# Optimization experiments

Hardware: AMD Instinct MI355X
Metric: run time of the kernel (lower is better)

The kernel has to match this reference:

```python
import math
import jax, jax.numpy as jnp
import numpy as np

B, T, D, L, E = 2, 1024, 1024, 12, 4
EPS = 1e-5


def _ln(v, g, b):
    mu = jnp.mean(v, axis=-1, keepdims=True)
    var = jnp.mean(jnp.square(v - mu), axis=-1, keepdims=True)
    return (v - mu) * jax.lax.rsqrt(var + EPS) * g + b


def setup_inputs() -> dict:
    key = jax.random.key(0)
    ks = jax.random.split(key, 4)
    x = jax.random.normal(ks[0], (B, T, D), dtype=jnp.float32)
    queries = jax.random.normal(ks[1], (L, D), dtype=jnp.float32) * 0.02
    W1 = jax.random.normal(ks[2], (L, D, E * D), dtype=jnp.float32) * 0.02
    W2 = jax.random.normal(ks[3], (L, E * D, D), dtype=jnp.float32) * 0.02
    return {
        'x': x,
        'queries': queries,
        'kn_g': jnp.ones((L, D), jnp.float32),
        'kn_b': jnp.zeros((L, D), jnp.float32),
        'ln_g': jnp.ones((L, D), jnp.float32),
        'ln_b': jnp.zeros((L, D), jnp.float32),
        'W1': W1,
        'b1': jnp.zeros((L, E * D), jnp.float32),
        'W2': W2,
        'b2': jnp.zeros((L, D), jnp.float32),
    }


def reference(x, queries, kn_g, kn_b, ln_g, ln_b, W1, b1, W2, b2):
    scale = 1.0 / math.sqrt(D)
    history = [x]
    h = x
    for l in range(L):
        V = jnp.stack(history, axis=0)              # (l+1, B, T, D)
        K = _ln(V, kn_g[l], kn_b[l])
        scores = jnp.einsum('d,lbtd->lbt', queries[l], K) * scale
        alpha = jax.nn.softmax(scores, axis=0)       # softmax over history axis
        residual = jnp.einsum('lbt,lbtd->btd', alpha, V)
        u = _ln(h, ln_g[l], ln_b[l])
        ff = jax.nn.gelu(u @ W1[l] + b1[l], approximate=False) @ W2[l] + b2[l]
        h = residual + ff
        history.append(h)
    return h
```

## Files before the change

kernel.cpp:

```cpp
#include <hip/hip_runtime.h>
#include <math.h>

#define BATCH 2
#define TSEQ 1024
#define DIM 1024
#define NLAYER 12
#define EDIM 4096
#define BT 2048
#define EPS_LN 1e-5f

typedef __attribute__((ext_vector_type(4))) float  f32x4;
typedef __attribute__((ext_vector_type(8))) __bf16 bf16x8;
typedef __attribute__((ext_vector_type(4))) __bf16 bf16x4;

__device__ __forceinline__ void gl_lds16(const void* gptr, void* lptr) {
    __builtin_amdgcn_global_load_lds(
        (const __attribute__((address_space(1))) void*)gptr,
        (__attribute__((address_space(3))) void*)lptr,
        16, 0, 0);
}

__global__ __launch_bounds__(256)
void attn_kernel(const float* __restrict__ x,
                 const float* __restrict__ hist,
                 const float* __restrict__ q,
                 const float* __restrict__ kng,
                 const float* __restrict__ knb,
                 const float* __restrict__ lng,
                 const float* __restrict__ lnb,
                 const float* __restrict__ b2,
                 float* __restrict__ hnext,
                 __bf16* __restrict__ u,
                 int nl)
{
    __shared__ float V[NLAYER][DIM];
    __shared__ float sS[NLAYER], sMu[NLAYER], sRs[NLAYER];

    const int bt = blockIdx.x;
    const int tid = threadIdx.x, lane = tid & 63, w = tid >> 6;

    f32x4 gqv[4];
    float sg = 0.f, sb = 0.f;
#pragma unroll
    for (int i = 0; i < 4; i++) {
        int d = i * 256 + lane * 4;
        f32x4 g4 = *(const f32x4*)(kng + d);
        f32x4 q4 = *(const f32x4*)(q + d);
        f32x4 b4 = *(const f32x4*)(knb + d);
#pragma unroll
        for (int c = 0; c < 4; c++) {
            float gq = g4[c] * q4[c];
            gqv[i][c] = gq;
            sg += gq;
            sb += b4[c] * q4[c];
        }
    }
#pragma unroll
    for (int off = 32; off; off >>= 1) {
        sg += __shfl_xor(sg, off);
        sb += __shfl_xor(sb, off);
    }

    for (int lp = w; lp < nl; lp += 4) {
        const float* vp = (lp == 0) ? (x + (size_t)bt * DIM)
                                    : (hist + ((size_t)lp * BT + bt) * DIM);
        f32x4 vv[4];
#pragma unroll
        for (int i = 0; i < 4; i++) vv[i] = *(const f32x4*)(vp + i * 256 + lane * 4);
        float s1 = 0.f, s2 = 0.f, sq = 0.f;
#pragma unroll
        for (int i = 0; i < 4; i++) {
            *(f32x4*)(&V[lp][i * 256 + lane * 4]) = vv[i];
#pragma unroll
            for (int c = 0; c < 4; c++) {
                float xv = vv[i][c];
                s1 += xv; s2 += xv * xv; sq += xv * gqv[i][c];
            }
        }
#pragma unroll
        for (int off = 32; off; off >>= 1) {
            s1 += __shfl_xor(s1, off);
            s2 += __shfl_xor(s2, off);
            sq += __shfl_xor(sq, off);
        }
        if (lane == 0) {
            float mu = s1 * (1.0f / DIM);
            float var = s2 * (1.0f / DIM) - mu * mu;
            float rs = rsqrtf(var + EPS_LN);
            sMu[lp] = mu; sRs[lp] = rs;
            sS[lp] = (rs * (sq - mu * sg) + sb) * (1.0f / 32.0f);
        }
    }
    __syncthreads();

    float mx = -1e30f;
#pragma unroll
    for (int i = 0; i < NLAYER; i++) if (i < nl) mx = fmaxf(mx, sS[i]);
    float al[NLAYER];
    float ssum = 0.f;
#pragma unroll
    for (int i = 0; i < NLAYER; i++) {
        al[i] = (i < nl) ? __expf(sS[i] - mx) : 0.f;
        ssum += al[i];
    }
    float inv = 1.0f / ssum;

    const int d = tid * 4;
    f32x4 r; r[0] = 0.f; r[1] = 0.f; r[2] = 0.f; r[3] = 0.f;
#pragma unroll
    for (int i = 0; i < NLAYER; i++) {
        if (i < nl) {
            f32x4 v4 = *(const f32x4*)(&V[i][d]);
            float a = al[i] * inv;
            r[0] += a * v4[0]; r[1] += a * v4[1]; r[2] += a * v4[2]; r[3] += a * v4[3];
        }
    }
    f32x4 h4 = *(const f32x4*)(&V[nl - 1][d]);
    f32x4 b24 = *(const f32x4*)(b2 + d);
    f32x4 ro; ro[0] = r[0] + b24[0]; ro[1] = r[1] + b24[1];
    ro[2] = r[2] + b24[2]; ro[3] = r[3] + b24[3];
    *(f32x4*)(hnext + (size_t)bt * DIM + d) = ro;

    float mu = sMu[nl - 1], rs = sRs[nl - 1];
    f32x4 g4 = *(const f32x4*)(lng + d);
    f32x4 b4 = *(const f32x4*)(lnb + d);
    bf16x4 uo;
#pragma unroll
    for (int c = 0; c < 4; c++) uo[c] = (__bf16)((h4[c] - mu) * rs * g4[c] + b4[c]);
    *(bf16x4*)(u + (size_t)bt * DIM + d) = uo;
}

__global__ __launch_bounds__(256) void wtrans_kernel(
    const float* __restrict__ W1, const float* __restrict__ W2,
    __bf16* __restrict__ W1t, __bf16* __restrict__ W2t)
{
    __shared__ float t[64][65];
    int z = blockIdx.z;
    const float* src; __bf16* dst; int R, C, rt, ct;
    if (z == 0) { src = W1; dst = W1t; R = DIM;  C = EDIM; rt = blockIdx.y; ct = blockIdx.x; }
    else        { src = W2; dst = W2t; R = EDIM; C = DIM;  rt = blockIdx.x; ct = blockIdx.y; }

    int tid = threadIdx.x;
    int lr = tid >> 2, cs = (tid & 3) << 4;
    const float* sp = src + (size_t)(rt * 64 + lr) * C + ct * 64 + cs;
#pragma unroll
    for (int s = 0; s < 4; s++) {
        f32x4 v = *(const f32x4*)(sp + s * 4);
        t[lr][cs + s * 4 + 0] = v[0];
        t[lr][cs + s * 4 + 1] = v[1];
        t[lr][cs + s * 4 + 2] = v[2];
        t[lr][cs + s * 4 + 3] = v[3];
    }
    __syncthreads();
    int oc = tid >> 2, rs = (tid & 3) << 4;
    bf16x8 o0, o1;
#pragma unroll
    for (int e = 0; e < 8; e++) o0[e] = (__bf16)t[rs + e][oc];
#pragma unroll
    for (int e = 0; e < 8; e++) o1[e] = (__bf16)t[rs + 8 + e][oc];
    __bf16* dp = dst + (size_t)(ct * 64 + oc) * R + rt * 64 + rs;
    *(bf16x8*)dp = o0;
    *(bf16x8*)(dp + 8) = o1;
}

#define STG 49152

template <int EPI, int NTN>
__global__ __launch_bounds__(512, 1)
void gemm8(const __bf16* __restrict__ A, const __bf16* __restrict__ Bt,
           const float* __restrict__ bias, float* __restrict__ outp,
           int N, int As, int Bs)
{
    __shared__ char lds[3 * STG];
    const int tid = threadIdx.x, lane = tid & 63, w = tid >> 6;
    const int wm = w >> 2, wn = w & 3;
    const int lr = lane & 15;
    const int hib = (lane >> 4) << 4;
    const int NT = 16;

    const int nb = gridDim.x;
    const int fid = blockIdx.x;
    const int swz = (fid & 7) * (nb >> 3) + (fid >> 3);
    const int m0 = (swz / NTN) * 128;
    const int n0 = (swz % NTN) * 256;
    const int kbase = blockIdx.y * 1024;

    f32x4 acc[4][4];
#pragma unroll
    for (int i = 0; i < 4; i++)
#pragma unroll
        for (int j = 0; j < 4; j++) { acc[i][j][0]=0.f; acc[i][j][1]=0.f; acc[i][j][2]=0.f; acc[i][j][3]=0.f; }

    const int srow = tid >> 3;
    const int ksrc = ((tid & 7) << 4) ^ ((srow & 7) << 4);
    const char* Ac = (const char*)A;
    const char* Bc = (const char*)Bt;
    size_t aoff[2], boff[4];
#pragma unroll
    for (int c = 0; c < 2; c++)
        aoff[c] = ((size_t)(m0 + c * 64 + srow) * As + kbase) * 2 + ksrc;
#pragma unroll
    for (int c = 0; c < 4; c++)
        boff[c] = ((size_t)(n0 + c * 64 + srow) * Bs + kbase) * 2 + ksrc;

    char* abw = lds + w * 1024;
    char* bbw = lds + 16384 + w * 1024;

    auto STAGE = [&](int tt, int bi) {
        size_t kb = (size_t)tt * 128;
        char* ab = abw + bi * STG;
        char* bb = bbw + bi * STG;
#pragma unroll
        for (int c = 0; c < 2; c++) gl_lds16(Ac + aoff[c] + kb, ab + c * 8192);
#pragma unroll
        for (int c = 0; c < 4; c++) gl_lds16(Bc + boff[c] + kb, bb + c * 8192);
    };

    STAGE(0, 0);
    STAGE(1, 1);

    int sb = 0, st = 2;
#pragma unroll 1
    for (int t = 0; t < NT; ++t) {
        if (t < NT - 1) asm volatile("s_waitcnt vmcnt(6)" ::: "memory");
        else            asm volatile("s_waitcnt vmcnt(0)" ::: "memory");
        __builtin_amdgcn_s_barrier();
        __builtin_amdgcn_sched_barrier(0);

        if (t + 2 < NT) STAGE(t + 2, st);

        const char* base = lds + sb * STG;
        bf16x8 af[2][4], bfr[2][4];
#pragma unroll
        for (int kk = 0; kk < 2; kk++) {
#pragma unroll
            for (int i = 0; i < 4; i++) {
                int ra = wm * 64 + i * 16 + lr;
                af[kk][i] = *(const bf16x8*)(base + ra * 128 + ((kk * 64 + hib) ^ ((ra & 7) << 4)));
            }
#pragma unroll
            for (int j = 0; j < 4; j++) {
                int rb = wn * 64 + j * 16 + lr;
                bfr[kk][j] = *(const bf16x8*)(base + 16384 + rb * 128 + ((kk * 64 + hib) ^ ((rb & 7) << 4)));
            }
        }
        __builtin_amdgcn_s_setprio(1);
#pragma unroll
        for (int kk = 0; kk < 2; kk++)
#pragma unroll
            for (int i = 0; i < 4; i++)
#pragma unroll
                for (int j = 0; j < 4; j++)
                    acc[i][j] = __builtin_amdgcn_mfma_f32_16x16x32_bf16(af[kk][i], bfr[kk][j], acc[i][j], 0, 0, 0);
        __builtin_amdgcn_s_setprio(0);

        sb = (sb == 2) ? 0 : sb + 1;
        st = (st == 2) ? 0 : st + 1;
    }

    const int lrow = (lane >> 4) << 2;
    if (EPI == 0) {
        __bf16* out = (__bf16*)outp;
#pragma unroll
        for (int i = 0; i < 4; i++) {
#pragma unroll
            for (int j = 0; j < 4; j++) {
                int colg = n0 + wn * 64 + j * 16 + lr;
                float bc = bias[colg];
#pragma unroll
                for (int r = 0; r < 4; r++) {
                    int rowg = m0 + wm * 64 + i * 16 + lrow + r;
                    float v = acc[i][j][r] + bc;
                    float tt2 = 0.7978845608f * (v + 0.044715f * v * v * v);
                    float e = __expf(2.0f * tt2);
                    float th = 1.0f - 2.0f / (e + 1.0f);
                    out[(size_t)rowg * N + colg] = (__bf16)(0.5f * v * (1.0f + th));
                }
            }
        }
    } else {
        float* out = outp + (size_t)blockIdx.y * BT * N;
#pragma unroll
        for (int i = 0; i < 4; i++) {
#pragma unroll
            for (int j = 0; j < 4; j++) {
                int colg = n0 + wn * 64 + j * 16 + lr;
#pragma unroll
                for (int r = 0; r < 4; r++) {
                    int rowg = m0 + wm * 64 + i * 16 + lrow + r;
                    out[(size_t)rowg * N + colg] = acc[i][j][r];
                }
            }
        }
    }
}

__global__ void reduce_kernel(const float* __restrict__ part, float* __restrict__ h)
{
    size_t i = ((size_t)blockIdx.x * 256 + threadIdx.x) * 4;
    f32x4 r = *(const f32x4*)(h + i);
#pragma unroll
    for (int z = 0; z < 4; z++) {
        f32x4 p = *(const f32x4*)(part + (size_t)z * BT * DIM + i);
        r[0] += p[0]; r[1] += p[1]; r[2] += p[2]; r[3] += p[3];
    }
    *(f32x4*)(h + i) = r;
}

extern "C" void kernel_launch(void* const* d_in, const int* in_sizes, int n_in,
                              void* d_out, int out_size, void* d_ws, size_t ws_size,
                              hipStream_t stream)
{
    const float* x   = (const float*)d_in[0];
    const float* q   = (const float*)d_in[1];
    const float* kng = (const float*)d_in[2];
    const float* knb = (const float*)d_in[3];
    const float* lng = (const float*)d_in[4];
    const float* lnb = (const float*)d_in[5];
    const float* W1  = (const float*)d_in[6];
    const float* b1  = (const float*)d_in[7];
    const float* W2  = (const float*)d_in[8];
    const float* b2  = (const float*)d_in[9];

    char* ws = (char*)d_ws;
    const size_t slot = (size_t)BT * DIM;
    float*  hist    = (float*)(ws);
    __bf16* ubuf    = (__bf16*)(ws + 109051904);
    __bf16* hmid    = (__bf16*)(ws + 113246208);
    __bf16* W1t     = (__bf16*)(ws + 130023424);
    __bf16* W2t     = (__bf16*)(ws + 138412032);
    float*  part    = (float*)(ws + 146800640);

    for (int l = 0; l < NLAYER; l++) {
        int nl = l + 1;
        wtrans_kernel<<<dim3(64, 16, 2), 256, 0, stream>>>(
            W1 + (size_t)l * DIM * EDIM, W2 + (size_t)l * EDIM * DIM, W1t, W2t);
        attn_kernel<<<dim3(BT), 256, 0, stream>>>(
            x, hist, q + (size_t)l * DIM,
            kng + (size_t)l * DIM, knb + (size_t)l * DIM,
            lng + (size_t)l * DIM, lnb + (size_t)l * DIM,
            b2 + (size_t)l * DIM,
            hist + (size_t)nl * slot, ubuf, nl);
        gemm8<0, 16><<<dim3(256, 1), 512, 0, stream>>>(
            ubuf, W1t, b1 + (size_t)l * EDIM, (float*)hmid, EDIM, DIM, DIM);
        gemm8<2, 4><<<dim3(64, 4), 512, 0, stream>>>(
            hmid, W2t, nullptr, part, DIM, EDIM, EDIM);
        reduce_kernel<<<dim3(BT * DIM / 1024), 256, 0, stream>>>(
            part, hist + (size_t)nl * slot);
    }

    hipMemcpyAsync(d_out, hist + (size_t)NLAYER * slot, slot * sizeof(float),
                   hipMemcpyDeviceToDevice, stream);
}
```

Before: 1.028 ms.

## Use 256x256 GEMM tiles and overlap next-layer weight transpose with GEMM1

The GEMM kernel moves from 128x256 to 256x256 tiles with a double-buffered LDS pipeline. Each wave now holds 8x4 accumulators and loads its A fragments in two halves. The per-layer weight transpose kernel is removed: extra blocks of the first GEMM transpose the next layer's W1/W2 into a ping-pong buffer while the 128 GEMM blocks compute. History slots shift by one, so the workspace shrinks. The aim is more operand reuse per LDS load and hiding the weight conversion. The risks are higher register pressure, the drop from three to two LDS stages, and a smaller grid for GEMM2.

```diff
diff --git a/kernel.cpp b/kernel.cpp
--- a/kernel.cpp
+++ b/kernel.cpp
@@ -63,7 +63,7 @@
 
     for (int lp = w; lp < nl; lp += 4) {
         const float* vp = (lp == 0) ? (x + (size_t)bt * DIM)
-                                    : (hist + ((size_t)lp * BT + bt) * DIM);
+                                    : (hist + ((size_t)(lp - 1) * BT + bt) * DIM);
         f32x4 vv[4];
 #pragma unroll
         for (int i = 0; i < 4; i++) vv[i] = *(const f32x4*)(vp + i * 256 + lane * 4);
@@ -163,31 +163,76 @@
     *(bf16x8*)(dp + 8) = o1;
 }
 
-#define STG 49152
-
-template <int EPI, int NTN>
+__device__ __forceinline__ void wtile(float (*t)[65], const float* src,
+                                      __bf16* dst, int R, int C,
+                                      int rt, int ct, int t256)
+{
+    int lr = t256 >> 2, cs = (t256 & 3) << 4;
+    const float* sp = src + (size_t)(rt * 64 + lr) * C + ct * 64 + cs;
+#pragma unroll
+    for (int s = 0; s < 4; s++) {
+        f32x4 v = *(const f32x4*)(sp + s * 4);
+        t[lr][cs + s * 4 + 0] = v[0];
+        t[lr][cs + s * 4 + 1] = v[1];
+        t[lr][cs + s * 4 + 2] = v[2];
+        t[lr][cs + s * 4 + 3] = v[3];
+    }
+    __syncthreads();
+    int oc = t256 >> 2, rs = (t256 & 3) << 4;
+    bf16x8 o0, o1;
+#pragma unroll
+    for (int e = 0; e < 8; e++) o0[e] = (__bf16)t[rs + e][oc];
+#pragma unroll
+    for (int e = 0; e < 8; e++) o1[e] = (__bf16)t[rs + 8 + e][oc];
+    __bf16* dp = dst + (size_t)(ct * 64 + oc) * R + rt * 64 + rs;
+    *(bf16x8*)dp = o0;
+    *(bf16x8*)(dp + 8) = o1;
+    __syncthreads();
+}
+
+template <int EPI, int NTN, int WT>
 __global__ __launch_bounds__(512, 1)
-void gemm8(const __bf16* __restrict__ A, const __bf16* __restrict__ Bt,
-           const float* __restrict__ bias, float* __restrict__ outp,
-           int N, int As, int Bs)
-{
-    __shared__ char lds[3 * STG];
+void gemm256(const __bf16* __restrict__ A, const __bf16* __restrict__ Bt,
+             const float* __restrict__ bias, float* __restrict__ outp,
+             int N, int As, int Bs,
+             const float* __restrict__ W1n, const float* __restrict__ W2n,
+             __bf16* __restrict__ W1tn, __bf16* __restrict__ W2tn, int dowt)
+{
+    __shared__ char lds[131072];
     const int tid = threadIdx.x, lane = tid & 63, w = tid >> 6;
+
+    if (WT && blockIdx.x >= 128) {
+        if (!dowt) return;
+        float (*tf)[65] = (float(*)[65])(lds) + (size_t)(tid >> 8) * 64;
+        int t256 = tid & 255;
+        int bid2 = blockIdx.x - 128;
+#pragma unroll 1
+        for (int uu = 0; uu < 8; uu++) {
+            int tile = (bid2 * 8 + uu) * 2 + (tid >> 8);
+            if (tile < 1024) {
+                wtile(tf, W1n, W1tn, DIM, EDIM, tile >> 6, tile & 63, t256);
+            } else {
+                int t2 = tile - 1024;
+                wtile(tf, W2n, W2tn, EDIM, DIM, t2 & 63, t2 >> 6, t256);
+            }
+        }
+        return;
+    }
+
     const int wm = w >> 2, wn = w & 3;
     const int lr = lane & 15;
     const int hib = (lane >> 4) << 4;
-    const int NT = 16;
-
-    const int nb = gridDim.x;
+
+    const int nb = WT ? 128 : gridDim.x;
     const int fid = blockIdx.x;
     const int swz = (fid & 7) * (nb >> 3) + (fid >> 3);
-    const int m0 = (swz / NTN) * 128;
+    const int m0 = (swz / NTN) * 256;
     const int n0 = (swz % NTN) * 256;
     const int kbase = blockIdx.y * 1024;
 
-    f32x4 acc[4][4];
-#pragma unroll
-    for (int i = 0; i < 4; i++)
+    f32x4 acc[8][4];
+#pragma unroll
+    for (int i = 0; i < 8; i++)
 #pragma unroll
         for (int j = 0; j < 4; j++) { acc[i][j][0]=0.f; acc[i][j][1]=0.f; acc[i][j][2]=0.f; acc[i][j][3]=0.f; }
 
@@ -195,81 +240,93 @@
     const int ksrc = ((tid & 7) << 4) ^ ((srow & 7) << 4);
     const char* Ac = (const char*)A;
     const char* Bc = (const char*)Bt;
-    size_t aoff[2], boff[4];
-#pragma unroll
-    for (int c = 0; c < 2; c++)
+    size_t aoff[4], boff[4];
+#pragma unroll
+    for (int c = 0; c < 4; c++) {
         aoff[c] = ((size_t)(m0 + c * 64 + srow) * As + kbase) * 2 + ksrc;
-#pragma unroll
-    for (int c = 0; c < 4; c++)
         boff[c] = ((size_t)(n0 + c * 64 + srow) * Bs + kbase) * 2 + ksrc;
-
-    char* abw = lds + w * 1024;
-    char* bbw = lds + 16384 + w * 1024;
-
-    auto STAGE = [&](int tt, int bi) {
+    }
+    char* ldsw = lds + w * 1024;
+
+    auto STAGE = [&](int tt, int p) {
         size_t kb = (size_t)tt * 128;
-        char* ab = abw + bi * STG;
-        char* bb = bbw + bi * STG;
-#pragma unroll
-        for (int c = 0; c < 2; c++) gl_lds16(Ac + aoff[c] + kb, ab + c * 8192);
-#pragma unroll
-        for (int c = 0; c < 4; c++) gl_lds16(Bc + boff[c] + kb, bb + c * 8192);
+        char* bb = ldsw + p * 65536;
+#pragma unroll
+        for (int c = 0; c < 4; c++) gl_lds16(Ac + aoff[c] + kb, bb + c * 8192);
+#pragma unroll
+        for (int c = 0; c < 4; c++) gl_lds16(Bc + boff[c] + kb, bb + 32768 + c * 8192);
     };
 
     STAGE(0, 0);
     STAGE(1, 1);
-
-    int sb = 0, st = 2;
+    asm volatile("s_waitcnt vmcnt(8)" ::: "memory");
+    __builtin_amdgcn_s_barrier();
+    __builtin_amdgcn_sched_barrier(0);
+
 #pragma unroll 1
-    for (int t = 0; t < NT; ++t) {
-        if (t < NT - 1) asm volatile("s_waitcnt vmcnt(6)" ::: "memory");
-        else            asm volatile("s_waitcnt vmcnt(0)" ::: "memory");
+    for (int t = 0; t < 16; ++t) {
+        const char* baseA = lds + (size_t)(t & 1) * 65536;
+        const char* baseB = baseA + 32768;
+#pragma unroll
+        for (int kk = 0; kk < 2; kk++) {
+            const int kb = kk * 64 + hib;
+            bf16x8 bfr[4];
+#pragma unroll
+            for (int j = 0; j < 4; j++) {
+                int rb = wn * 64 + j * 16 + lr;
+                bfr[j] = *(const bf16x8*)(baseB + rb * 128 + (kb ^ ((rb & 7) << 4)));
+            }
+            bf16x8 afr[4];
+#pragma unroll
+            for (int i2 = 0; i2 < 4; i2++) {
+                int ra = wm * 128 + i2 * 16 + lr;
+                afr[i2] = *(const bf16x8*)(baseA + ra * 128 + (kb ^ ((ra & 7) << 4)));
+            }
+            __builtin_amdgcn_s_setprio(1);
+#pragma unroll
+            for (int i2 = 0; i2 < 4; i2++)
+#pragma unroll
+                for (int j = 0; j < 4; j++)
+                    acc[i2][j] = __builtin_amdgcn_mfma_f32_16x16x32_bf16(afr[i2], bfr[j], acc[i2][j], 0, 0, 0);
+            __builtin_amdgcn_s_setprio(0);
+#pragma unroll
+            for (int i2 = 0; i2 < 4; i2++) {
+                int ra = wm * 128 + (i2 + 4) * 16 + lr;
+                afr[i2] = *(const bf16x8*)(baseA + ra * 128 + (kb ^ ((ra & 7) << 4)));
+            }
+            __builtin_amdgcn_s_setprio(1);
+#pragma unroll
+            for (int i2 = 0; i2 < 4; i2++)
+#pragma unroll
+                for (int j = 0; j < 4; j++)
+                    acc[i2 + 4][j] = __builtin_amdgcn_mfma_f32_16x16x32_bf16(afr[i2], bfr[j], acc[i2 + 4][j], 0, 0, 0);
+            __builtin_amdgcn_s_setprio(0);
+        }
+        __builtin_amdgcn_sched_barrier(0);
         __builtin_amdgcn_s_barrier();
         __builtin_amdgcn_sched_barrier(0);
-
-        if (t + 2 < NT) STAGE(t + 2, st);
-
-        const char* base = lds + sb * STG;
-        bf16x8 af[2][4], bfr[2][4];
-#pragma unroll
-        for (int kk = 0; kk < 2; kk++) {
-#pragma unroll
-            for (int i = 0; i < 4; i++) {
-                int ra = wm * 64 + i * 16 + lr;
-                af[kk][i] = *(const bf16x8*)(base + ra * 128 + ((kk * 64 + hib) ^ ((ra & 7) << 4)));
-            }
-#pragma unroll
-            for (int j = 0; j < 4; j++) {
-                int rb = wn * 64 + j * 16 + lr;
-                bfr[kk][j] = *(const bf16x8*)(base + 16384 + rb * 128 + ((kk * 64 + hib) ^ ((rb & 7) << 4)));
-            }
-        }
-        __builtin_amdgcn_s_setprio(1);
-#pragma unroll
-        for (int kk = 0; kk < 2; kk++)
-#pragma unroll
-            for (int i = 0; i < 4; i++)
-#pragma unroll
-                for (int j = 0; j < 4; j++)
-                    acc[i][j] = __builtin_amdgcn_mfma_f32_16x16x32_bf16(af[kk][i], bfr[kk][j], acc[i][j], 0, 0, 0);
-        __builtin_amdgcn_s_setprio(0);
-
-        sb = (sb == 2) ? 0 : sb + 1;
-        st = (st == 2) ? 0 : st + 1;
+        if (t + 2 < 16) {
+            STAGE(t + 2, t & 1);
+            asm volatile("s_waitcnt vmcnt(8)" ::: "memory");
+        } else {
+            asm volatile("s_waitcnt vmcnt(0)" ::: "memory");
+        }
+        __builtin_amdgcn_s_barrier();
+        __builtin_amdgcn_sched_barrier(0);
     }
 
     const int lrow = (lane >> 4) << 2;
     if (EPI == 0) {
         __bf16* out = (__bf16*)outp;
 #pragma unroll
-        for (int i = 0; i < 4; i++) {
+        for (int i = 0; i < 8; i++) {
 #pragma unroll
             for (int j = 0; j < 4; j++) {
                 int colg = n0 + wn * 64 + j * 16 + lr;
                 float bc = bias[colg];
 #pragma unroll
                 for (int r = 0; r < 4; r++) {
-                    int rowg = m0 + wm * 64 + i * 16 + lrow + r;
+                    int rowg = m0 + wm * 128 + i * 16 + lrow + r;
                     float v = acc[i][j][r] + bc;
                     float tt2 = 0.7978845608f * (v + 0.044715f * v * v * v);
                     float e = __expf(2.0f * tt2);
@@ -281,13 +338,13 @@
     } else {
         float* out = outp + (size_t)blockIdx.y * BT * N;
 #pragma unroll
-        for (int i = 0; i < 4; i++) {
+        for (int i = 0; i < 8; i++) {
 #pragma unroll
             for (int j = 0; j < 4; j++) {
                 int colg = n0 + wn * 64 + j * 16 + lr;
 #pragma unroll
                 for (int r = 0; r < 4; r++) {
-                    int rowg = m0 + wm * 64 + i * 16 + lrow + r;
+                    int rowg = m0 + wm * 128 + i * 16 + lrow + r;
                     out[(size_t)rowg * N + colg] = acc[i][j][r];
                 }
             }
@@ -324,31 +381,36 @@
 
     char* ws = (char*)d_ws;
     const size_t slot = (size_t)BT * DIM;
-    float*  hist    = (float*)(ws);
-    __bf16* ubuf    = (__bf16*)(ws + 109051904);
-    __bf16* hmid    = (__bf16*)(ws + 113246208);
-    __bf16* W1t     = (__bf16*)(ws + 130023424);
-    __bf16* W2t     = (__bf16*)(ws + 138412032);
-    float*  part    = (float*)(ws + 146800640);
+    float*  hist  = (float*)(ws);
+    __bf16* ubuf  = (__bf16*)(ws + 100663296);
+    __bf16* hmid  = (__bf16*)(ws + 104857600);
+    __bf16* W1tb[2] = { (__bf16*)(ws + 121634816), (__bf16*)(ws + 130023424) };
+    __bf16* W2tb[2] = { (__bf16*)(ws + 138412032), (__bf16*)(ws + 146800640) };
+    float*  part  = (float*)(ws + 155189248);
+
+    wtrans_kernel<<<dim3(64, 16, 2), 256, 0, stream>>>(W1, W2, W1tb[0], W2tb[0]);
 
     for (int l = 0; l < NLAYER; l++) {
         int nl = l + 1;
-        wtrans_kernel<<<dim3(64, 16, 2), 256, 0, stream>>>(
-            W1 + (size_t)l * DIM * EDIM, W2 + (size_t)l * EDIM * DIM, W1t, W2t);
+        int ln = (l + 1 < NLAYER) ? l + 1 : l;
+        float* hnext = hist + (size_t)l * slot;
         attn_kernel<<<dim3(BT), 256, 0, stream>>>(
             x, hist, q + (size_t)l * DIM,
             kng + (size_t)l * DIM, knb + (size_t)l * DIM,
             lng + (size_t)l * DIM, lnb + (size_t)l * DIM,
-            b2 + (size_t)l * DIM,
-            hist + (size_t)nl * slot, ubuf, nl);
-        gemm8<0, 16><<<dim3(256, 1), 512, 0, stream>>>(
-            ubuf, W1t, b1 + (size_t)l * EDIM, (float*)hmid, EDIM, DIM, DIM);
-        gemm8<2, 4><<<dim3(64, 4), 512, 0, stream>>>(
-            hmid, W2t, nullptr, part, DIM, EDIM, EDIM);
-        reduce_kernel<<<dim3(BT * DIM / 1024), 256, 0, stream>>>(
-            part, hist + (size_t)nl * slot);
-    }
-
-    hipMemcpyAsync(d_out, hist + (size_t)NLAYER * slot, slot * sizeof(float),
+            b2 + (size_t)l * DIM, hnext, ubuf, nl);
+        gemm256<0, 16, 1><<<dim3(256, 1), 512, 0, stream>>>(
+            ubuf, W1tb[l & 1], b1 + (size_t)l * EDIM, (float*)hmid,
+            EDIM, DIM, DIM,
+            W1 + (size_t)ln * DIM * EDIM, W2 + (size_t)ln * EDIM * DIM,
+            W1tb[(l + 1) & 1], W2tb[(l + 1) & 1], (l + 1 < NLAYER) ? 1 : 0);
+        gemm256<2, 4, 0><<<dim3(32, 4), 512, 0, stream>>>(
+            hmid, W2tb[l & 1], nullptr, part,
+            DIM, EDIM, EDIM,
+            nullptr, nullptr, nullptr, nullptr, 0);
+        reduce_kernel<<<dim3(BT * DIM / 1024), 256, 0, stream>>>(part, hnext);
+    }
+
+    hipMemcpyAsync(d_out, hist + (size_t)(NLAYER - 1) * slot, slot * sizeof(float),
                    hipMemcpyDeviceToDevice, stream);
 }
```

Result: slower. 1.252 ms (+21.7%).

## Fuse next-layer weight transpose into attention kernel and atomically reduce split-K

Applied to the files above, without the earlier changes.

Folds the per-layer weight transpose/bf16 conversion for the next layer into the attention kernel as extra blocks, using double-buffered transposed weight slots. Only the first layer's transpose stays a separate launch. The second GEMM's split-K partials are now accumulated into the history slot with atomic adds instead of written to a partial buffer and summed by a separate reduce kernel. History indexing shifts by one slot. This removes two launches per layer and the partial-buffer traffic, at the cost of atomic contention and non-deterministic summation order.

```diff
diff --git a/kernel.cpp b/kernel.cpp
--- a/kernel.cpp
+++ b/kernel.cpp
@@ -20,21 +20,75 @@
         16, 0, 0);
 }
 
+__device__ __forceinline__ void wtile256(float (*t)[65], const float* src,
+                                         __bf16* dst, int R, int C,
+                                         int rt, int ct, int tid)
+{
+    int lr = tid >> 2, cs = (tid & 3) << 4;
+    const float* sp = src + (size_t)(rt * 64 + lr) * C + ct * 64 + cs;
+#pragma unroll
+    for (int s = 0; s < 4; s++) {
+        f32x4 v = *(const f32x4*)(sp + s * 4);
+        t[lr][cs + s * 4 + 0] = v[0];
+        t[lr][cs + s * 4 + 1] = v[1];
+        t[lr][cs + s * 4 + 2] = v[2];
+        t[lr][cs + s * 4 + 3] = v[3];
+    }
+    __syncthreads();
+    int oc = tid >> 2, rs = (tid & 3) << 4;
+    bf16x8 o0, o1;
+#pragma unroll
+    for (int e = 0; e < 8; e++) o0[e] = (__bf16)t[rs + e][oc];
+#pragma unroll
+    for (int e = 0; e < 8; e++) o1[e] = (__bf16)t[rs + 8 + e][oc];
+    __bf16* dp = dst + (size_t)(ct * 64 + oc) * R + rt * 64 + rs;
+    *(bf16x8*)dp = o0;
+    *(bf16x8*)(dp + 8) = o1;
+}
+
+__global__ __launch_bounds__(256) void wtrans_kernel(
+    const float* __restrict__ W1, const float* __restrict__ W2,
+    __bf16* __restrict__ W1t, __bf16* __restrict__ W2t)
+{
+    __shared__ float t[64][65];
+    int z = blockIdx.z;
+    if (z == 0) wtile256(t, W1, W1t, DIM, EDIM, blockIdx.y, blockIdx.x, threadIdx.x);
+    else        wtile256(t, W2, W2t, EDIM, DIM, blockIdx.x, blockIdx.y, threadIdx.x);
+}
+
 __global__ __launch_bounds__(256)
-void attn_kernel(const float* __restrict__ x,
-                 const float* __restrict__ hist,
-                 const float* __restrict__ q,
-                 const float* __restrict__ kng,
-                 const float* __restrict__ knb,
-                 const float* __restrict__ lng,
-                 const float* __restrict__ lnb,
-                 const float* __restrict__ b2,
-                 float* __restrict__ hnext,
-                 __bf16* __restrict__ u,
-                 int nl)
-{
-    __shared__ float V[NLAYER][DIM];
-    __shared__ float sS[NLAYER], sMu[NLAYER], sRs[NLAYER];
+void attn_wt_kernel(const float* __restrict__ x,
+                    const float* __restrict__ hist,
+                    const float* __restrict__ q,
+                    const float* __restrict__ kng,
+                    const float* __restrict__ knb,
+                    const float* __restrict__ lng,
+                    const float* __restrict__ lnb,
+                    const float* __restrict__ b2,
+                    float* __restrict__ hnext,
+                    __bf16* __restrict__ u,
+                    int nl,
+                    const float* __restrict__ W1n,
+                    const float* __restrict__ W2n,
+                    __bf16* __restrict__ W1tn,
+                    __bf16* __restrict__ W2tn,
+                    int dowt)
+{
+    __shared__ char smem[49408];
+
+    if (blockIdx.x >= BT) {
+        if (!dowt) return;
+        float (*t)[65] = (float(*)[65])smem;
+        int tile = blockIdx.x - BT;
+        if (tile < 1024) wtile256(t, W1n, W1tn, DIM, EDIM, tile >> 6, tile & 63, threadIdx.x);
+        else { int t3 = tile - 1024; wtile256(t, W2n, W2tn, EDIM, DIM, t3 & 63, t3 >> 6, threadIdx.x); }
+        return;
+    }
+
+    float (*V)[DIM] = (float(*)[DIM])smem;
+    float* sS  = (float*)(smem + 49152);
+    float* sMu = sS + NLAYER;
+    float* sRs = sMu + NLAYER;
 
     const int bt = blockIdx.x;
     const int tid = threadIdx.x, lane = tid & 63, w = tid >> 6;
@@ -63,7 +117,7 @@
 
     for (int lp = w; lp < nl; lp += 4) {
         const float* vp = (lp == 0) ? (x + (size_t)bt * DIM)
-                                    : (hist + ((size_t)lp * BT + bt) * DIM);
+                                    : (hist + ((size_t)(lp - 1) * BT + bt) * DIM);
         f32x4 vv[4];
 #pragma unroll
         for (int i = 0; i < 4; i++) vv[i] = *(const f32x4*)(vp + i * 256 + lane * 4);
@@ -128,39 +182,6 @@
 #pragma unroll
     for (int c = 0; c < 4; c++) uo[c] = (__bf16)((h4[c] - mu) * rs * g4[c] + b4[c]);
     *(bf16x4*)(u + (size_t)bt * DIM + d) = uo;
-}
-
-__global__ __launch_bounds__(256) void wtrans_kernel(
-    const float* __restrict__ W1, const float* __restrict__ W2,
-    __bf16* __restrict__ W1t, __bf16* __restrict__ W2t)
-{
-    __shared__ float t[64][65];
-    int z = blockIdx.z;
-    const float* src; __bf16* dst; int R, C, rt, ct;
-    if (z == 0) { src = W1; dst = W1t; R = DIM;  C = EDIM; rt = blockIdx.y; ct = blockIdx.x; }
-    else        { src = W2; dst = W2t; R = EDIM; C = DIM;  rt = blockIdx.x; ct = blockIdx.y; }
-
-    int tid = threadIdx.x;
-    int lr = tid >> 2, cs = (tid & 3) << 4;
-    const float* sp = src + (size_t)(rt * 64 + lr) * C + ct * 64 + cs;
-#pragma unroll
-    for (int s = 0; s < 4; s++) {
-        f32x4 v = *(const f32x4*)(sp + s * 4);
-        t[lr][cs + s * 4 + 0] = v[0];
-        t[lr][cs + s * 4 + 1] = v[1];
-        t[lr][cs + s * 4 + 2] = v[2];
-        t[lr][cs + s * 4 + 3] = v[3];
-    }
-    __syncthreads();
-    int oc = tid >> 2, rs = (tid & 3) << 4;
-    bf16x8 o0, o1;
-#pragma unroll
-    for (int e = 0; e < 8; e++) o0[e] = (__bf16)t[rs + e][oc];
-#pragma unroll
-    for (int e = 0; e < 8; e++) o1[e] = (__bf16)t[rs + 8 + e][oc];
-    __bf16* dp = dst + (size_t)(ct * 64 + oc) * R + rt * 64 + rs;
-    *(bf16x8*)dp = o0;
-    *(bf16x8*)(dp + 8) = o1;
 }
 
 #define STG 49152
@@ -279,7 +300,7 @@
             }
         }
     } else {
-        float* out = outp + (size_t)blockIdx.y * BT * N;
+        float* out = outp;
 #pragma unroll
         for (int i = 0; i < 4; i++) {
 #pragma unroll
@@ -288,23 +309,11 @@
 #pragma unroll
                 for (int r = 0; r < 4; r++) {
                     int rowg = m0 + wm * 64 + i * 16 + lrow + r;
-                    out[(size_t)rowg * N + colg] = acc[i][j][r];
+                    unsafeAtomicAdd(&out[(size_t)rowg * N + colg], acc[i][j][r]);
                 }
             }
         }
     }
-}
-
-__global__ void reduce_kernel(const float* __restrict__ part, float* __restrict__ h)
-{
-    size_t i = ((size_t)blockIdx.x * 256 + threadIdx.x) * 4;
-    f32x4 r = *(const f32x4*)(h + i);
-#pragma unroll
-    for (int z = 0; z < 4; z++) {
-        f32x4 p = *(const f32x4*)(part + (size_t)z * BT * DIM + i);
-        r[0] += p[0]; r[1] += p[1]; r[2] += p[2]; r[3] += p[3];
-    }
-    *(f32x4*)(h + i) = r;
 }
 
 extern "C" void kernel_launch(void* const* d_in, const int* in_sizes, int n_in,
@@ -324,31 +333,31 @@
 
     char* ws = (char*)d_ws;
     const size_t slot = (size_t)BT * DIM;
-    float*  hist    = (float*)(ws);
-    __bf16* ubuf    = (__bf16*)(ws + 109051904);
-    __bf16* hmid    = (__bf16*)(ws + 113246208);
-    __bf16* W1t     = (__bf16*)(ws + 130023424);
-    __bf16* W2t     = (__bf16*)(ws + 138412032);
-    float*  part    = (float*)(ws + 146800640);
+    float*  hist  = (float*)(ws);
+    __bf16* ubuf  = (__bf16*)(ws + 100663296);
+    __bf16* hmid  = (__bf16*)(ws + 104857600);
+    __bf16* W1tb[2] = { (__bf16*)(ws + 121634816), (__bf16*)(ws + 130023424) };
+    __bf16* W2tb[2] = { (__bf16*)(ws + 138412032), (__bf16*)(ws + 146800640) };
+
+    wtrans_kernel<<<dim3(64, 16, 2), 256, 0, stream>>>(W1, W2, W1tb[0], W2tb[0]);
 
     for (int l = 0; l < NLAYER; l++) {
         int nl = l + 1;
-        wtrans_kernel<<<dim3(64, 16, 2), 256, 0, stream>>>(
-            W1 + (size_t)l * DIM * EDIM, W2 + (size_t)l * EDIM * DIM, W1t, W2t);
-        attn_kernel<<<dim3(BT), 256, 0, stream>>>(
+        int ln = (l + 1 < NLAYER) ? l + 1 : l;
+        float* hnext = hist + (size_t)l * slot;
+        attn_wt_kernel<<<dim3(2 * BT), 256, 0, stream>>>(
             x, hist, q + (size_t)l * DIM,
             kng + (size_t)l * DIM, knb + (size_t)l * DIM,
             lng + (size_t)l * DIM, lnb + (size_t)l * DIM,
-            b2 + (size_t)l * DIM,
-            hist + (size_t)nl * slot, ubuf, nl);
+            b2 + (size_t)l * DIM, hnext, ubuf, nl,
+            W1 + (size_t)ln * DIM * EDIM, W2 + (size_t)ln * EDIM * DIM,
+            W1tb[(l + 1) & 1], W2tb[(l + 1) & 1], (l + 1 < NLAYER) ? 1 : 0);
         gemm8<0, 16><<<dim3(256, 1), 512, 0, stream>>>(
-            ubuf, W1t, b1 + (size_t)l * EDIM, (float*)hmid, EDIM, DIM, DIM);
+            ubuf, W1tb[l & 1], b1 + (size_t)l * EDIM, (float*)hmid, EDIM, DIM, DIM);
         gemm8<2, 4><<<dim3(64, 4), 512, 0, stream>>>(
-            hmid, W2t, nullptr, part, DIM, EDIM, EDIM);
-        reduce_kernel<<<dim3(BT * DIM / 1024), 256, 0, stream>>>(
-            part, hist + (size_t)nl * slot);
-    }
-
-    hipMemcpyAsync(d_out, hist + (size_t)NLAYER * slot, slot * sizeof(float),
+            hmid, W2tb[l & 1], nullptr, hnext, DIM, EDIM, EDIM);
+    }
+
+    hipMemcpyAsync(d_out, hist + (size_t)(NLAYER - 1) * slot, slot * sizeof(float),
                    hipMemcpyDeviceToDevice, stream);
 }
```

Measured after the change: 1.113 ms. 8.3% more time.
